# Kernel tuning notes

Hardware: AMD Instinct MI355X
Metric: run time of the kernel (lower is better)

Reference implementation:

```python
import jax, jax.numpy as jnp
import numpy as np
from jax import lax

B, L, D_MODEL = 4, 1024, 512
D_STATE, D_CONV, D_INNER = 16, 4, 2 * D_MODEL


def setup_inputs() -> dict:
    key = jax.random.key(0)
    ks = jax.random.split(key, 8)
    s = 0.02
    x = jax.random.normal(ks[0], (B, L, D_MODEL), dtype=jnp.float32)
    W_in = jax.random.normal(ks[1], (D_MODEL, 2 * D_INNER), dtype=jnp.float32) * s
    conv_w = jax.random.normal(ks[2], (D_INNER, 1, D_CONV), dtype=jnp.float32) * s  # OIH, depthwise
    conv_b = jnp.zeros((D_INNER,), jnp.float32)
    W_x = jax.random.normal(ks[3], (D_INNER, 2 * D_STATE), dtype=jnp.float32) * s
    W_dt = jax.random.normal(ks[4], (D_INNER, D_INNER), dtype=jnp.float32) * s
    b_dt = jnp.zeros((D_INNER,), jnp.float32)
    # A_log = -logspace(log10(0.001), log10(1.0), d_state); used directly as A in the scan
    A_log = -jnp.logspace(np.log10(1e-3), 0.0, D_STATE, dtype=jnp.float32)
    D_skip = jnp.ones((D_INNER,), jnp.float32) * 0.1
    W_out = jax.random.normal(ks[5], (D_INNER, D_MODEL), dtype=jnp.float32) * s
    gamma = jnp.ones((D_MODEL,), jnp.float32)
    beta = jnp.zeros((D_MODEL,), jnp.float32)
    return dict(x=x, W_in=W_in, conv_w=conv_w, conv_b=conv_b, W_x=W_x, W_dt=W_dt,
                b_dt=b_dt, A_log=A_log, D_skip=D_skip, W_out=W_out, gamma=gamma, beta=beta)


def _mamba_forward(x, W_in, conv_w, conv_b, W_x, W_dt, b_dt, A_log, D_skip, W_out, gamma, beta):
    x = jnp.clip(x, -10.0, 10.0)
    x_and_res = x @ W_in                                  # [B, L, 2*d_inner]
    xp, res = jnp.split(x_and_res, 2, axis=-1)
    # Depthwise causal conv1d: torch pads d_conv-1 both sides then slices [:L] -> left-pad only.
    xt = jnp.transpose(xp, (0, 2, 1))                     # [B, d_inner, L]
    xc = lax.conv_general_dilated(xt, conv_w, window_strides=(1,),
                                  padding=[(D_CONV - 1, 0)],
                                  dimension_numbers=('NCH', 'OIH', 'NCH'),
                                  feature_group_count=D_INNER)
    xc = xc + conv_b[None, :, None]
    xc = jax.nn.silu(jnp.transpose(xc, (0, 2, 1)))        # [B, L, d_inner]
    ssm = xc @ W_x                                        # [B, L, 2*d_state]
    Bm, Cm = jnp.split(ssm, 2, axis=-1)                   # each [B, L, d_state]
    delta = xc @ W_dt + b_dt                              # [B, L, d_inner] (no softplus in source)

    # Selective scan over time (sequential recurrence)
    def step(h, inp):
        u_t, d_t, B_t, C_t = inp                          # [B,I], [B,I], [B,S], [B,S]
        dA = jnp.exp(jnp.clip(d_t[:, :, None] * A_log, -5.0, 5.0))   # [B, I, S]
        h = dA * h + (d_t[:, :, None] * B_t[:, None, :]) * u_t[:, :, None]
        y = jnp.einsum('bis,bs->bi', h, C_t)
        return h, y

    tm = lambda a: jnp.swapaxes(a, 0, 1)                  # time-major
    h0 = jnp.zeros((x.shape[0], D_INNER, D_STATE), xc.dtype)
    _, ys = lax.scan(step, h0, (tm(xc), tm(delta), tm(Bm), tm(Cm)))
    y = jnp.swapaxes(ys, 0, 1) + xc * D_skip              # D skip connection

    y = y * jax.nn.silu(res)                              # gating
    out = y @ W_out
    r = out + x                                           # residual
    mu = jnp.mean(r, axis=-1, keepdims=True)
    var = jnp.var(r, axis=-1, keepdims=True)
    return gamma * (r - mu) / jnp.sqrt(var + 1e-5) + beta


def reference(x, W_in, conv_w, conv_b, W_x, W_dt, b_dt, A_log, D_skip, W_out, gamma, beta):
    return _mamba_forward(x, W_in, conv_w, conv_b, W_x, W_dt, b_dt, A_log, D_skip, W_out, gamma, beta)
```

## Files before the change

### kernel.cpp

```cpp
#include <hip/hip_runtime.h>
#include <hip/hip_bf16.h>

typedef __hip_bfloat16 bf16;
typedef unsigned short ushort_t;
typedef unsigned int uint_t;
typedef __attribute__((ext_vector_type(8))) __bf16 bf16x8;
typedef __attribute__((ext_vector_type(4))) float f32x4;

#define BB 4
#define LL 1024
#define DM 512
#define DS 16
#define DI 1024
#define ROWS 4096
#define NC 64
#define CT 16
#define NDTX 1152

__device__ __forceinline__ float b2f(bf16 v) { return __bfloat162float(v); }

__device__ __forceinline__ float load_flag(const void* src, int i, int isbf)
{
    return isbf ? b2f(((const bf16*)src)[i]) : ((const float*)src)[i];
}

__device__ __forceinline__ ushort_t f2b_bits(float v)
{
    bf16 t = __float2bfloat16(v);
    return *(ushort_t*)&t;
}

__device__ __forceinline__ int detect_local(const ushort_t* wdt)
{
    __shared__ int bad;
    if (threadIdx.x == 0) bad = 0;
    __syncthreads();
    ushort_t u = wdt[threadIdx.x];
    if (((u >> 7) & 0xFF) >= 127) atomicAdd(&bad, 1);
    __syncthreads();
    return (bad <= 8) ? 1 : 0;
}

__global__ __launch_bounds__(256)
void prep_all(const void* x, const void* Win, const void* Wdt, const void* Wx,
              const void* Wout, const void* cw, const void* cb, const void* Alog,
              const void* Dsk, const void* gam, const void* bet, const void* bdt,
              bf16* __restrict__ xbf, bf16* __restrict__ WtIn,
              bf16* __restrict__ WtDtx, bf16* __restrict__ WtOut,
              float* __restrict__ ccw, float* __restrict__ ccb,
              float* __restrict__ cAlg, float* __restrict__ cDsk,
              float* __restrict__ cgam, float* __restrict__ cbet,
              float* __restrict__ bdtx)
{
    const int isbf = detect_local((const ushort_t*)Wdt);
    int blk = blockIdx.x;

    if (blk < 2048) {
        int idx = blk * 256 + threadIdx.x;
        float v[4];
        if (isbf) {
            uint2 raw = ((const uint2*)x)[idx];
            v[0] = __uint_as_float(raw.x << 16);
            v[1] = __uint_as_float(raw.x & 0xFFFF0000u);
            v[2] = __uint_as_float(raw.y << 16);
            v[3] = __uint_as_float(raw.y & 0xFFFF0000u);
        } else {
            float4 raw = ((const float4*)x)[idx];
            v[0] = raw.x; v[1] = raw.y; v[2] = raw.z; v[3] = raw.w;
        }
        uint_t b0, b1;
        b0 = f2b_bits(fminf(fmaxf(v[0], -10.f), 10.f))
           | ((uint_t)f2b_bits(fminf(fmaxf(v[1], -10.f), 10.f)) << 16);
        b1 = f2b_bits(fminf(fmaxf(v[2], -10.f), 10.f))
           | ((uint_t)f2b_bits(fminf(fmaxf(v[3], -10.f), 10.f)) << 16);
        uint2 ow; ow.x = b0; ow.y = b1;
        ((uint2*)xbf)[idx] = ow;
    } else if (blk < 4640) {
        int tb = blk - 2048;
        const void* src; bf16* dst; int K, Nsrc, tpr;
        if (tb < 1024)      { src = Win;  dst = WtIn;               K = 512;  Nsrc = 2048; tpr = 64; }
        else if (tb < 2048) { tb -= 1024; src = Wdt;  dst = WtDtx;  K = 1024; Nsrc = 1024; tpr = 32; }
        else if (tb < 2080) { tb -= 2048; src = Wx;   dst = WtDtx + 1024 * 1024; K = 1024; Nsrc = 32; tpr = 1; }
        else                { tb -= 2080; src = Wout; dst = WtOut;  K = 1024; Nsrc = 512;  tpr = 16; }
        int k0 = (tb / tpr) * 32, n0 = (tb % tpr) * 32;

        __shared__ float tile[32][33];
        int tx = threadIdx.x & 31, ty = threadIdx.x >> 5;
        #pragma unroll
        for (int j = 0; j < 4; ++j)
            tile[ty + 8 * j][tx] = load_flag(src, (k0 + ty + 8 * j) * Nsrc + n0 + tx, isbf);
        __syncthreads();
        #pragma unroll
        for (int j = 0; j < 4; ++j)
            dst[(size_t)(n0 + ty + 8 * j) * K + k0 + tx] = __float2bfloat16(tile[tx][ty + 8 * j]);
    } else {
        int i = (blk - 4640) * 256 + threadIdx.x;
        if (i < 4096)        ccw[i] = load_flag(cw, i, isbf);
        else if (i < 5120)   ccb[i - 4096] = load_flag(cb, i - 4096, isbf);
        else if (i < 5136)   cAlg[i - 5120] = load_flag(Alog, i - 5120, isbf);
        else if (i < 6160)   cDsk[i - 5136] = load_flag(Dsk, i - 5136, isbf);
        else if (i < 6672)   cgam[i - 6160] = load_flag(gam, i - 6160, isbf);
        else if (i < 7184)   cbet[i - 6672] = load_flag(bet, i - 6672, isbf);
        else if (i < 8336) {
            int j = i - 7184;
            bdtx[j] = (j < DI) ? load_flag(bdt, j, isbf) : 0.f;
        } else if (i < 106640) {
            (WtDtx + 1056 * 1024)[i - 8336] = __float2bfloat16(0.f);
        }
    }
}

__device__ __forceinline__ void gload16(const bf16* g, ushort_t* l)
{
    __builtin_amdgcn_global_load_lds(
        (const __attribute__((address_space(1))) void*)g,
        (__attribute__((address_space(3))) void*)l, 16, 0, 0);
}

template <int TM, int TN, bool OBF>
__global__ __launch_bounds__(256)
void gemm_mfma(const bf16* __restrict__ A, const bf16* __restrict__ Bt,
               const float* __restrict__ bias, void* __restrict__ Cv,
               int M, int N, int K)
{
    constexpr int MI = TM / 32, NJ = TN / 32;
    constexpr int NLD = (TM + TN) / 64;
    __shared__ ushort_t As[TM * 32];
    __shared__ ushort_t Bs[TN * 32];

    const int tid = threadIdx.x;
    const int lane = tid & 63;
    const int w = tid >> 6;
    const int wr = w >> 1, wc = w & 1;
    const int m0 = blockIdx.y * TM;
    const int n0 = blockIdx.x * TN;

    const bf16* gptr[NLD];
    ushort_t* lbase[NLD];
    #pragma unroll
    for (int q = 0; q < NLD; ++q) {
        int p = q * 256 + tid;
        if (q * 256 < TM * 4) {
            int row = p >> 2, kc = ((p & 3) - row) & 3;
            gptr[q] = A + (size_t)(m0 + row) * K + kc * 8;
            lbase[q] = &As[(q * 256 + w * 64) * 8];
        } else {
            int pb = p - TM * 4;
            int row = pb >> 2, kc = ((pb & 3) - row) & 3;
            gptr[q] = Bt + (size_t)(n0 + row) * K + kc * 8;
            lbase[q] = &Bs[(q * 256 + w * 64 - TM * 4) * 8];
        }
    }

    f32x4 acc[MI][NJ];
    #pragma unroll
    for (int i = 0; i < MI; ++i)
        #pragma unroll
        for (int j = 0; j < NJ; ++j)
            acc[i][j] = (f32x4){0.f, 0.f, 0.f, 0.f};

    const int ko = lane >> 4;
    const int ml = lane & 15;

    for (int k0 = 0; k0 < K; k0 += 32) {
        #pragma unroll
        for (int q = 0; q < NLD; ++q)
            gload16(gptr[q] + k0, lbase[q]);
        __syncthreads();

        bf16x8 af[MI], bfr[NJ];
        #pragma unroll
        for (int i = 0; i < MI; ++i) {
            int m = wr * (TM / 2) + i * 16 + ml;
            af[i] = *(const bf16x8*)&As[(m * 4 + ((ko + m) & 3)) * 8];
        }
        #pragma unroll
        for (int j = 0; j < NJ; ++j) {
            int n = wc * (TN / 2) + j * 16 + ml;
            bfr[j] = *(const bf16x8*)&Bs[(n * 4 + ((ko + n) & 3)) * 8];
        }
        #pragma unroll
        for (int i = 0; i < MI; ++i)
            #pragma unroll
            for (int j = 0; j < NJ; ++j)
                acc[i][j] = __builtin_amdgcn_mfma_f32_16x16x32_bf16(
                    af[i], bfr[j], acc[i][j], 0, 0, 0);
        __syncthreads();
    }

    const int rq = lane >> 4;
    #pragma unroll
    for (int j = 0; j < NJ; ++j) {
        int n = n0 + wc * (TN / 2) + j * 16 + ml;
        float bv = bias ? bias[n] : 0.f;
        #pragma unroll
        for (int i = 0; i < MI; ++i) {
            int mb = m0 + wr * (TM / 2) + i * 16 + rq * 4;
            #pragma unroll
            for (int r = 0; r < 4; ++r) {
                float v = acc[i][j][r] + bv;
                if (OBF) ((bf16*)Cv)[(size_t)(mb + r) * N + n] = __float2bfloat16(v);
                else     ((float*)Cv)[(size_t)(mb + r) * N + n] = v;
            }
        }
    }
}

__global__ __launch_bounds__(256)
void conv_silu(const bf16* __restrict__ xrb, const float* __restrict__ cw,
               const float* __restrict__ cb, bf16* __restrict__ xcb)
{
    int idx = blockIdx.x * 256 + threadIdx.x;
    int i = idx & (DI - 1);
    int row = idx >> 10;
    int t = row & (LL - 1);

    float w0 = cw[i * 4 + 0];
    float w1 = cw[i * 4 + 1];
    float w2 = cw[i * 4 + 2];
    float w3 = cw[i * 4 + 3];

    float acc = cb[i];
    const bf16* base = xrb + (size_t)row * 2048 + i;
    if (t >= 3) acc = fmaf(b2f(base[-3 * 2048]), w0, acc);
    if (t >= 2) acc = fmaf(b2f(base[-2 * 2048]), w1, acc);
    if (t >= 1) acc = fmaf(b2f(base[-1 * 2048]), w2, acc);
    acc = fmaf(b2f(base[0]), w3, acc);

    xcb[idx] = __float2bfloat16(acc / (1.f + __expf(-acc)));
}

__global__ __launch_bounds__(64)
void scan_chunk_summary(const bf16* __restrict__ xcb, const bf16* __restrict__ dlx,
                        const float* __restrict__ A_log,
                        bf16* __restrict__ P, bf16* __restrict__ Q)
{
    const int b = blockIdx.z, c = blockIdx.y;
    const int i = blockIdx.x * 64 + threadIdx.x;

    float a[DS];
    #pragma unroll
    for (int s = 0; s < DS; ++s) a[s] = A_log[s];
    float h[DS] = {};
    float p[DS];
    #pragma unroll
    for (int s = 0; s < DS; ++s) p[s] = 1.f;

    const int row0 = b * LL + c * CT;
    for (int t = 0; t < CT; ++t) {
        const size_t row = row0 + t;
        float d = b2f(dlx[row * NDTX + i]);
        float u = b2f(xcb[row * DI + i]);
        const bf16* sp = dlx + row * NDTX + 1024;
        #pragma unroll
        for (int s = 0; s < DS; ++s) {
            float e = fminf(fmaxf(d * a[s], -5.f), 5.f);
            float dA = __expf(e);
            h[s] = fmaf(dA, h[s], (d * b2f(sp[s])) * u);
            p[s] *= dA;
        }
    }
    #pragma unroll
    for (int s = 0; s < DS; ++s) {
        size_t idx = ((size_t)((b * NC + c) * DS + s)) * DI + i;
        P[idx] = __float2bfloat16(p[s]);
        Q[idx] = __float2bfloat16(h[s]);
    }
}

__global__ __launch_bounds__(256)
void scan_chunk_combine(const bf16* __restrict__ P, const bf16* __restrict__ Q,
                        bf16* __restrict__ HS)
{
    int n = blockIdx.x * 256 + threadIdx.x;
    int i = n & (DI - 1);
    int s = (n >> 10) & (DS - 1);
    int b = n >> 14;
    float h = 0.f;
    for (int c = 0; c < NC; ++c) {
        size_t idx = ((size_t)((b * NC + c) * DS + s)) * DI + i;
        HS[idx] = __float2bfloat16(h);
        h = fmaf(b2f(P[idx]), h, b2f(Q[idx]));
    }
}

__global__ __launch_bounds__(64)
void scan_chunk_apply(const bf16* __restrict__ xcb, const bf16* __restrict__ dlx,
                      const bf16* __restrict__ xrb, const float* __restrict__ A_log,
                      const float* __restrict__ Dskip, const bf16* __restrict__ HS,
                      bf16* __restrict__ ybf)
{
    const int b = blockIdx.z, c = blockIdx.y;
    const int i = blockIdx.x * 64 + threadIdx.x;

    float a[DS];
    #pragma unroll
    for (int s = 0; s < DS; ++s) a[s] = A_log[s];
    float h[DS];
    #pragma unroll
    for (int s = 0; s < DS; ++s)
        h[s] = b2f(HS[((size_t)((b * NC + c) * DS + s)) * DI + i]);
    const float dsk = Dskip[i];

    const int row0 = b * LL + c * CT;
    for (int t = 0; t < CT; ++t) {
        const size_t row = row0 + t;
        float d = b2f(dlx[row * NDTX + i]);
        float u = b2f(xcb[row * DI + i]);
        const bf16* sp = dlx + row * NDTX + 1024;
        float y = 0.f;
        #pragma unroll
        for (int s = 0; s < DS; ++s) {
            float e = fminf(fmaxf(d * a[s], -5.f), 5.f);
            float dA = __expf(e);
            h[s] = fmaf(dA, h[s], (d * b2f(sp[s])) * u);
            y = fmaf(h[s], b2f(sp[DS + s]), y);
        }
        float res = b2f(xrb[row * 2048 + DI + i]);
        float g = res / (1.f + __expf(-res));
        ybf[row * DI + i] = __float2bfloat16((y + u * dsk) * g);
    }
}

__global__ __launch_bounds__(256)
void ln_kernel(const float* __restrict__ outp, const void* __restrict__ xsrc,
               const void* __restrict__ wdt_probe,
               const float* __restrict__ gamma, const float* __restrict__ beta,
               void* __restrict__ out)
{
    const int isbf = detect_local((const ushort_t*)wdt_probe);
    const int row = blockIdx.x;
    const int tid = threadIdx.x;

    float r[2];
    float sum = 0.f, ss = 0.f;
    #pragma unroll
    for (int q = 0; q < 2; ++q) {
        int j = tid + q * 256;
        float xv = load_flag(xsrc, row * DM + j, isbf);
        xv = fminf(fmaxf(xv, -10.f), 10.f);
        float v = outp[(size_t)row * DM + j] + xv;
        r[q] = v;
        sum += v;
        ss = fmaf(v, v, ss);
    }
    #pragma unroll
    for (int off = 32; off >= 1; off >>= 1) {
        sum += __shfl_down(sum, off);
        ss  += __shfl_down(ss, off);
    }
    __shared__ float s1[4], s2[4];
    __shared__ float stats[2];
    int wid = tid >> 6, lane = tid & 63;
    if (lane == 0) { s1[wid] = sum; s2[wid] = ss; }
    __syncthreads();
    if (tid == 0) {
        float S = s1[0] + s1[1] + s1[2] + s1[3];
        float Qq = s2[0] + s2[1] + s2[2] + s2[3];
        float mean = S / DM;
        float var = Qq / DM - mean * mean;
        stats[0] = mean;
        stats[1] = rsqrtf(var + 1e-5f);
    }
    __syncthreads();
    float mean = stats[0], rstd = stats[1];
    #pragma unroll
    for (int q = 0; q < 2; ++q) {
        int j = tid + q * 256;
        float v = (r[q] - mean) * rstd * gamma[j] + beta[j];
        size_t o = (size_t)row * DM + j;
        if (isbf) ((bf16*)out)[o] = __float2bfloat16(v);
        else      ((float*)out)[o] = v;
    }
}

extern "C" void kernel_launch(void* const* d_in, const int* in_sizes, int n_in,
                              void* d_out, int out_size, void* d_ws, size_t ws_size,
                              hipStream_t stream)
{
    float* W = (float*)d_ws;
    float* ccw  = W;
    float* ccb  = ccw  + 4096;
    float* cAlg = ccb  + 1024;
    float* cDsk = cAlg + 16;
    float* cgam = cDsk + 1024;
    float* cbet = cgam + 512;
    float* bdtx = cbet + 512;
    float* outp = bdtx + 1152;
    bf16*  xbf  = (bf16*)(outp + 2097152);
    bf16*  xrb  = xbf  + 2097152;
    bf16*  xcb  = xrb  + 8388608;
    bf16*  ybf  = xcb  + 4194304;
    bf16*  dlx  = ybf  + 4194304;
    bf16*  Pbuf = dlx  + 4718592;
    bf16*  Qbuf = Pbuf + 4194304;
    bf16*  HS   = Qbuf + 4194304;
    bf16*  WtIn = HS   + 4194304;
    bf16*  WtDtx= WtIn + 1048576;
    bf16*  WtOut= WtDtx+ 1179648;

    prep_all<<<5057, 256, 0, stream>>>(
        d_in[0], d_in[1], d_in[5], d_in[4], d_in[9], d_in[2], d_in[3],
        d_in[7], d_in[8], d_in[10], d_in[11], d_in[6],
        xbf, WtIn, WtDtx, WtOut, ccw, ccb, cAlg, cDsk, cgam, cbet, bdtx);

    gemm_mfma<64, 128, true><<<dim3(2048 / 128, ROWS / 64), 256, 0, stream>>>(
        xbf, WtIn, nullptr, xrb, ROWS, 2048, 512);

    conv_silu<<<ROWS * DI / 256, 256, 0, stream>>>(xrb, ccw, ccb, xcb);

    gemm_mfma<64, 128, true><<<dim3(NDTX / 128, ROWS / 64), 256, 0, stream>>>(
        xcb, WtDtx, bdtx, dlx, ROWS, NDTX, DI);

    scan_chunk_summary<<<dim3(DI / 64, NC, BB), 64, 0, stream>>>(
        xcb, dlx, cAlg, Pbuf, Qbuf);
    scan_chunk_combine<<<BB * DS * DI / 256, 256, 0, stream>>>(Pbuf, Qbuf, HS);
    scan_chunk_apply<<<dim3(DI / 64, NC, BB), 64, 0, stream>>>(
        xcb, dlx, xrb, cAlg, cDsk, HS, ybf);

    gemm_mfma<64, 64, false><<<dim3(DM / 64, ROWS / 64), 256, 0, stream>>>(
        ybf, WtOut, nullptr, outp, ROWS, DM, DI);

    ln_kernel<<<ROWS, 256, 0, stream>>>(outp, d_in[0], d_in[5], cgam, cbet, d_out);
}
```

Before: 234.0 us.

## Fuse three-pass chunked scan into one kernel and widen GEMM K-tile

The chunk-summary, cross-chunk combine and apply kernels of the selective scan are merged into one 1024-thread kernel. Each block holds 16 channels across all 64 chunks and passes chunk states through LDS instead of global P/Q/HS buffers. This removes two launches and the global round-trips for chunk summaries, and keeps d and u in registers between passes. The grid drops to 256 blocks with heavy register use, and the combine step runs on only 256 threads. The GEMM also moves from a K-step of 32 to 64 with an 8-way swizzle, halving the barrier count per tile at the cost of doubling LDS per block.

New measurement: 226.4 us. 1.03x faster.

```diff
diff --git a/kernel.cpp b/kernel.cpp
--- a/kernel.cpp
+++ b/kernel.cpp
@@ -30,12 +30,18 @@
     return *(ushort_t*)&t;
 }
 
+__device__ __forceinline__ float bits2f(ushort_t u)
+{
+    uint_t w = ((uint_t)u) << 16;
+    return __uint_as_float(w);
+}
+
 __device__ __forceinline__ int detect_local(const ushort_t* wdt)
 {
     __shared__ int bad;
     if (threadIdx.x == 0) bad = 0;
     __syncthreads();
-    ushort_t u = wdt[threadIdx.x];
+    ushort_t u = wdt[threadIdx.x & 255];
     if (((u >> 7) & 0xFF) >= 127) atomicAdd(&bad, 1);
     __syncthreads();
     return (bad <= 8) ? 1 : 0;
@@ -124,9 +130,10 @@
                int M, int N, int K)
 {
     constexpr int MI = TM / 32, NJ = TN / 32;
-    constexpr int NLD = (TM + TN) / 64;
-    __shared__ ushort_t As[TM * 32];
-    __shared__ ushort_t Bs[TN * 32];
+    constexpr int NQA = TM * 8 / 256;
+    constexpr int NQB = TN * 8 / 256;
+    __shared__ ushort_t As[TM * 64];
+    __shared__ ushort_t Bs[TN * 64];
 
     const int tid = threadIdx.x;
     const int lane = tid & 63;
@@ -135,21 +142,21 @@
     const int m0 = blockIdx.y * TM;
     const int n0 = blockIdx.x * TN;
 
-    const bf16* gptr[NLD];
-    ushort_t* lbase[NLD];
-    #pragma unroll
-    for (int q = 0; q < NLD; ++q) {
+    const bf16* gA[NQA]; ushort_t* lA[NQA];
+    #pragma unroll
+    for (int q = 0; q < NQA; ++q) {
         int p = q * 256 + tid;
-        if (q * 256 < TM * 4) {
-            int row = p >> 2, kc = ((p & 3) - row) & 3;
-            gptr[q] = A + (size_t)(m0 + row) * K + kc * 8;
-            lbase[q] = &As[(q * 256 + w * 64) * 8];
-        } else {
-            int pb = p - TM * 4;
-            int row = pb >> 2, kc = ((pb & 3) - row) & 3;
-            gptr[q] = Bt + (size_t)(n0 + row) * K + kc * 8;
-            lbase[q] = &Bs[(q * 256 + w * 64 - TM * 4) * 8];
-        }
+        int row = p >> 3, kc = ((p & 7) - row) & 7;
+        gA[q] = A + (size_t)(m0 + row) * K + kc * 8;
+        lA[q] = &As[(q * 256 + w * 64) * 8];
+    }
+    const bf16* gB[NQB]; ushort_t* lB[NQB];
+    #pragma unroll
+    for (int q = 0; q < NQB; ++q) {
+        int p = q * 256 + tid;
+        int row = p >> 3, kc = ((p & 7) - row) & 7;
+        gB[q] = Bt + (size_t)(n0 + row) * K + kc * 8;
+        lB[q] = &Bs[(q * 256 + w * 64) * 8];
     }
 
     f32x4 acc[MI][NJ];
@@ -162,29 +169,33 @@
     const int ko = lane >> 4;
     const int ml = lane & 15;
 
-    for (int k0 = 0; k0 < K; k0 += 32) {
-        #pragma unroll
-        for (int q = 0; q < NLD; ++q)
-            gload16(gptr[q] + k0, lbase[q]);
+    for (int k0 = 0; k0 < K; k0 += 64) {
+        #pragma unroll
+        for (int q = 0; q < NQA; ++q) gload16(gA[q] + k0, lA[q]);
+        #pragma unroll
+        for (int q = 0; q < NQB; ++q) gload16(gB[q] + k0, lB[q]);
         __syncthreads();
 
-        bf16x8 af[MI], bfr[NJ];
-        #pragma unroll
-        for (int i = 0; i < MI; ++i) {
-            int m = wr * (TM / 2) + i * 16 + ml;
-            af[i] = *(const bf16x8*)&As[(m * 4 + ((ko + m) & 3)) * 8];
-        }
-        #pragma unroll
-        for (int j = 0; j < NJ; ++j) {
-            int n = wc * (TN / 2) + j * 16 + ml;
-            bfr[j] = *(const bf16x8*)&Bs[(n * 4 + ((ko + n) & 3)) * 8];
-        }
-        #pragma unroll
-        for (int i = 0; i < MI; ++i)
+        #pragma unroll
+        for (int half = 0; half < 2; ++half) {
+            bf16x8 af[MI], bfr[NJ];
             #pragma unroll
-            for (int j = 0; j < NJ; ++j)
-                acc[i][j] = __builtin_amdgcn_mfma_f32_16x16x32_bf16(
-                    af[i], bfr[j], acc[i][j], 0, 0, 0);
+            for (int i = 0; i < MI; ++i) {
+                int m = wr * (TM / 2) + i * 16 + ml;
+                af[i] = *(const bf16x8*)&As[(m * 8 + ((half * 4 + ko + m) & 7)) * 8];
+            }
+            #pragma unroll
+            for (int j = 0; j < NJ; ++j) {
+                int n = wc * (TN / 2) + j * 16 + ml;
+                bfr[j] = *(const bf16x8*)&Bs[(n * 8 + ((half * 4 + ko + n) & 7)) * 8];
+            }
+            #pragma unroll
+            for (int i = 0; i < MI; ++i)
+                #pragma unroll
+                for (int j = 0; j < NJ; ++j)
+                    acc[i][j] = __builtin_amdgcn_mfma_f32_16x16x32_bf16(
+                        af[i], bfr[j], acc[i][j], 0, 0, 0);
+        }
         __syncthreads();
     }
 
@@ -230,95 +241,88 @@
     xcb[idx] = __float2bfloat16(acc / (1.f + __expf(-acc)));
 }
 
-__global__ __launch_bounds__(64)
-void scan_chunk_summary(const bf16* __restrict__ xcb, const bf16* __restrict__ dlx,
-                        const float* __restrict__ A_log,
-                        bf16* __restrict__ P, bf16* __restrict__ Q)
-{
-    const int b = blockIdx.z, c = blockIdx.y;
-    const int i = blockIdx.x * 64 + threadIdx.x;
+__global__ __launch_bounds__(1024)
+void scan_fused(const bf16* __restrict__ xcb, const bf16* __restrict__ dlx,
+                const bf16* __restrict__ xrb, const float* __restrict__ A_log,
+                const float* __restrict__ Dskip, bf16* __restrict__ ybf)
+{
+    __shared__ ushort_t lp[NC * 16 * DS];
+    __shared__ ushort_t lq[NC * 16 * DS];
+
+    const int b = blockIdx.x >> 6;
+    const int ch0 = (blockIdx.x & 63) << 4;
+    const int chl = threadIdx.x & 15;
+    const int c = threadIdx.x >> 4;
+    const int i = ch0 + chl;
 
     float a[DS];
     #pragma unroll
     for (int s = 0; s < DS; ++s) a[s] = A_log[s];
+
+    const int row0 = b * LL + c * CT;
+    float d[CT], u[CT];
     float h[DS] = {};
     float p[DS];
     #pragma unroll
     for (int s = 0; s < DS; ++s) p[s] = 1.f;
 
-    const int row0 = b * LL + c * CT;
     for (int t = 0; t < CT; ++t) {
         const size_t row = row0 + t;
-        float d = b2f(dlx[row * NDTX + i]);
-        float u = b2f(xcb[row * DI + i]);
+        d[t] = b2f(dlx[row * NDTX + i]);
+        u[t] = b2f(xcb[row * DI + i]);
         const bf16* sp = dlx + row * NDTX + 1024;
         #pragma unroll
         for (int s = 0; s < DS; ++s) {
-            float e = fminf(fmaxf(d * a[s], -5.f), 5.f);
+            float e = fminf(fmaxf(d[t] * a[s], -5.f), 5.f);
             float dA = __expf(e);
-            h[s] = fmaf(dA, h[s], (d * b2f(sp[s])) * u);
+            h[s] = fmaf(dA, h[s], (d[t] * b2f(sp[s])) * u[t]);
             p[s] *= dA;
         }
     }
-    #pragma unroll
-    for (int s = 0; s < DS; ++s) {
-        size_t idx = ((size_t)((b * NC + c) * DS + s)) * DI + i;
-        P[idx] = __float2bfloat16(p[s]);
-        Q[idx] = __float2bfloat16(h[s]);
-    }
-}
-
-__global__ __launch_bounds__(256)
-void scan_chunk_combine(const bf16* __restrict__ P, const bf16* __restrict__ Q,
-                        bf16* __restrict__ HS)
-{
-    int n = blockIdx.x * 256 + threadIdx.x;
-    int i = n & (DI - 1);
-    int s = (n >> 10) & (DS - 1);
-    int b = n >> 14;
-    float h = 0.f;
-    for (int c = 0; c < NC; ++c) {
-        size_t idx = ((size_t)((b * NC + c) * DS + s)) * DI + i;
-        HS[idx] = __float2bfloat16(h);
-        h = fmaf(b2f(P[idx]), h, b2f(Q[idx]));
-    }
-}
-
-__global__ __launch_bounds__(64)
-void scan_chunk_apply(const bf16* __restrict__ xcb, const bf16* __restrict__ dlx,
-                      const bf16* __restrict__ xrb, const float* __restrict__ A_log,
-                      const float* __restrict__ Dskip, const bf16* __restrict__ HS,
-                      bf16* __restrict__ ybf)
-{
-    const int b = blockIdx.z, c = blockIdx.y;
-    const int i = blockIdx.x * 64 + threadIdx.x;
-
-    float a[DS];
-    #pragma unroll
-    for (int s = 0; s < DS; ++s) a[s] = A_log[s];
-    float h[DS];
-    #pragma unroll
-    for (int s = 0; s < DS; ++s)
-        h[s] = b2f(HS[((size_t)((b * NC + c) * DS + s)) * DI + i]);
+    {
+        const int off = (c * 16 + chl) * DS;
+        #pragma unroll
+        for (int s = 0; s < DS; ++s) {
+            lp[off + s] = f2b_bits(p[s]);
+            lq[off + s] = f2b_bits(h[s]);
+        }
+    }
+    __syncthreads();
+
+    if (threadIdx.x < 256) {
+        int cl = threadIdx.x & 15;
+        int s = threadIdx.x >> 4;
+        float hh = 0.f;
+        for (int cc = 0; cc < NC; ++cc) {
+            int off = (cc * 16 + cl) * DS + s;
+            float pp = bits2f(lp[off]);
+            float qq = bits2f(lq[off]);
+            lp[off] = f2b_bits(hh);
+            hh = fmaf(pp, hh, qq);
+        }
+    }
+    __syncthreads();
+
+    {
+        const int off = (c * 16 + chl) * DS;
+        #pragma unroll
+        for (int s = 0; s < DS; ++s) h[s] = bits2f(lp[off + s]);
+    }
     const float dsk = Dskip[i];
-
-    const int row0 = b * LL + c * CT;
     for (int t = 0; t < CT; ++t) {
         const size_t row = row0 + t;
-        float d = b2f(dlx[row * NDTX + i]);
-        float u = b2f(xcb[row * DI + i]);
         const bf16* sp = dlx + row * NDTX + 1024;
         float y = 0.f;
         #pragma unroll
         for (int s = 0; s < DS; ++s) {
-            float e = fminf(fmaxf(d * a[s], -5.f), 5.f);
+            float e = fminf(fmaxf(d[t] * a[s], -5.f), 5.f);
             float dA = __expf(e);
-            h[s] = fmaf(dA, h[s], (d * b2f(sp[s])) * u);
+            h[s] = fmaf(dA, h[s], (d[t] * b2f(sp[s])) * u[t]);
             y = fmaf(h[s], b2f(sp[DS + s]), y);
         }
         float res = b2f(xrb[row * 2048 + DI + i]);
         float g = res / (1.f + __expf(-res));
-        ybf[row * DI + i] = __float2bfloat16((y + u * dsk) * g);
+        ybf[row * DI + i] = __float2bfloat16((y + u[t] * dsk) * g);
     }
 }
 
@@ -392,10 +396,7 @@
     bf16*  xcb  = xrb  + 8388608;
     bf16*  ybf  = xcb  + 4194304;
     bf16*  dlx  = ybf  + 4194304;
-    bf16*  Pbuf = dlx  + 4718592;
-    bf16*  Qbuf = Pbuf + 4194304;
-    bf16*  HS   = Qbuf + 4194304;
-    bf16*  WtIn = HS   + 4194304;
+    bf16*  WtIn = dlx  + 4718592;
     bf16*  WtDtx= WtIn + 1048576;
     bf16*  WtOut= WtDtx+ 1179648;
 
@@ -412,11 +413,7 @@
     gemm_mfma<64, 128, true><<<dim3(NDTX / 128, ROWS / 64), 256, 0, stream>>>(
         xcb, WtDtx, bdtx, dlx, ROWS, NDTX, DI);
 
-    scan_chunk_summary<<<dim3(DI / 64, NC, BB), 64, 0, stream>>>(
-        xcb, dlx, cAlg, Pbuf, Qbuf);
-    scan_chunk_combine<<<BB * DS * DI / 256, 256, 0, stream>>>(Pbuf, Qbuf, HS);
-    scan_chunk_apply<<<dim3(DI / 64, NC, BB), 64, 0, stream>>>(
-        xcb, dlx, xrb, cAlg, cDsk, HS, ybf);
+    scan_fused<<<256, 1024, 0, stream>>>(xcb, dlx, xrb, cAlg, cDsk, ybf);
 
     gemm_mfma<64, 64, false><<<dim3(DM / 64, ROWS / 64), 256, 0, stream>>>(
         ybf, WtOut, nullptr, outp, ROWS, DM, DI);
```
